# Kernel optimization log

Hardware: AMD Instinct MI355X
Metric: run time of the kernel (lower is better)

The kernel has to match this reference:

```python
import jax, jax.numpy as jnp
import numpy as np

N_NODES = 50000
N_EDGES = 800000
IN_CH = 128
HID = 32
HEADS = 4
OUT_CH = 64
N_GRAPHS = 64


def setup_inputs() -> dict:
    key = jax.random.key(0)
    ks = jax.random.split(key, 16)
    x = jax.random.normal(ks[0], (N_NODES, IN_CH), dtype=jnp.float32)
    edge_index = jax.random.randint(ks[1], (2, N_EDGES), 0, N_NODES, dtype=jnp.int64)
    edge_attr = jax.random.normal(ks[2], (N_EDGES, 8), dtype=jnp.float32)
    nodeIDs = jnp.sort(jax.random.randint(ks[3], (N_NODES,), 0, N_GRAPHS, dtype=jnp.int64))
    s = 0.1
    W1 = jax.random.normal(ks[4], (IN_CH, HEADS * HID), dtype=jnp.float32) * s
    att_src1 = jax.random.normal(ks[5], (HEADS, HID), dtype=jnp.float32) * s
    att_dst1 = jax.random.normal(ks[6], (HEADS, HID), dtype=jnp.float32) * s
    b1 = jax.random.normal(ks[7], (HEADS * HID,), dtype=jnp.float32) * s
    W2 = jax.random.normal(ks[8], (HEADS * HID, 16), dtype=jnp.float32) * s
    att_src2 = jax.random.normal(ks[9], (1, 16), dtype=jnp.float32) * s
    att_dst2 = jax.random.normal(ks[10], (1, 16), dtype=jnp.float32) * s
    b2 = jax.random.normal(ks[11], (16,), dtype=jnp.float32) * s
    Wf = jax.random.normal(ks[12], (16, OUT_CH), dtype=jnp.float32) * s
    bf = jax.random.normal(ks[13], (OUT_CH,), dtype=jnp.float32) * s
    return dict(x=x, edge_index=edge_index, edge_attr=edge_attr, nodeIDs=nodeIDs,
                W1=W1, att_src1=att_src1, att_dst1=att_dst1, b1=b1,
                W2=W2, att_src2=att_src2, att_dst2=att_dst2, b2=b2,
                Wf=Wf, bf=bf)


def gat_conv(x, src, dst, n, W, a_src, a_dst, b, heads, out_ch, concat):
    # linear transform -> [N, H, C]
    h = (x @ W).reshape(n, heads, out_ch)
    # per-node attention logits [N, H]
    asrc = jnp.sum(h * a_src, axis=-1)
    adst = jnp.sum(h * a_dst, axis=-1)
    e = jax.nn.leaky_relu(asrc[src] + adst[dst], 0.2)  # [E, H]
    # segment softmax over edges sharing the same destination node
    m = jax.ops.segment_max(e, dst, num_segments=n)
    e = jnp.exp(e - m[dst])
    s = jax.ops.segment_sum(e, dst, num_segments=n)
    alpha = e / (s[dst] + 1e-16)
    # weighted scatter-add aggregation: [N, H, C]
    out = jax.ops.segment_sum(alpha[:, :, None] * h[src], dst, num_segments=n)
    out = out.reshape(n, heads * out_ch) if concat else out.mean(axis=1)
    return out + b


def reference(x, edge_index, edge_attr, nodeIDs, W1, att_src1, att_dst1, b1,
              W2, att_src2, att_dst2, b2, Wf, bf):
    n = x.shape[0]
    # GATConv default: add self-loops
    loop = jnp.arange(n, dtype=edge_index.dtype)
    src = jnp.concatenate([edge_index[0], loop])
    dst = jnp.concatenate([edge_index[1], loop])
    # eval mode: dropout is identity. edge_attr ignored (no edge_dim in GATConv).
    h = jax.nn.relu(gat_conv(x, src, dst, n, W1, att_src1, att_dst1, b1, HEADS, HID, True))
    h = jax.nn.relu(gat_conv(h, src, dst, n, W2, att_src2, att_dst2, b2, 1, 16, False))
    # global mean pool over graphs
    sums = jax.ops.segment_sum(h, nodeIDs, num_segments=N_GRAPHS)
    cnts = jax.ops.segment_sum(jnp.ones((n,), dtype=h.dtype), nodeIDs, num_segments=N_GRAPHS)
    pooled = sums / jnp.maximum(cnts, 1.0)[:, None]  # [G, 16]
    return pooled @ Wf + bf
```

## Files before the change

### kernel.cpp

```cpp
#include <hip/hip_runtime.h>
#include <hip/hip_bf16.h>


__device__ __forceinline__ float lrelu02(float x) { return x > 0.f ? x : 0.2f * x; }

__device__ __forceinline__ unsigned short f2bf(float f) {
    unsigned b = __float_as_uint(f);
    return (unsigned short)((b + 0x7fffu + ((b >> 16) & 1u)) >> 16);
}
__device__ __forceinline__ float bf_lo(unsigned u) { return __uint_as_float(u << 16); }
__device__ __forceinline__ float bf_hi(unsigned u) { return __uint_as_float(u & 0xffff0000u); }

typedef __attribute__((ext_vector_type(8))) short short8v;
typedef __attribute__((ext_vector_type(4))) float f32x4;

#define CAP 64

__global__ __launch_bounds__(128) void k_prep(
    const float* __restrict__ W1, unsigned short* __restrict__ W1tb)
{
    int n = blockIdx.x, k = threadIdx.x;
    W1tb[n * 128 + k] = f2bf(W1[k * 128 + n]);
}

__global__ __launch_bounds__(256) void k_gemm1h(
    const float* __restrict__ x, const unsigned short* __restrict__ W1tb,
    const float* __restrict__ a_src, const float* __restrict__ a_dst,
    unsigned short* __restrict__ H1b, float* __restrict__ asrcv, float* __restrict__ adstv, int N,
    const int* __restrict__ src, const int* __restrict__ dst,
    int* __restrict__ cnt, unsigned short* __restrict__ bkt, int E, int GB)
{
    if ((int)blockIdx.x >= GB) {
        const int g  = blockIdx.x & 7;
        const int lo = (int)(((long long)N * g) >> 3);
        const int hi = (int)(((long long)N * (g + 1)) >> 3);
        const int bi = (blockIdx.x - GB) >> 3;
        for (int i = bi * 256 + threadIdx.x; i < E; i += 128 * 256) {
            int d = dst[i];
            if (d >= lo && d < hi) {
                int slot = atomicAdd(&cnt[d], 1);
                if (slot < CAP) bkt[(d << 6) + slot] = (unsigned short)src[i];
            }
        }
        return;
    }

    __shared__ unsigned short sL[4][16][136];
    const int tid = threadIdx.x;
    const int w  = tid >> 6, l = tid & 63;
    const int mr = l & 15, kg = l >> 4;
    const int m0 = w * 16;
    const int rowbase = blockIdx.x * 64;

    const int grow_a = rowbase + m0 + mr;
    const float* xr = x + (size_t)(grow_a < N ? grow_a : N - 1) * 128;

    f32x4 acc[8];
#pragma unroll
    for (int nt = 0; nt < 8; ++nt) acc[nt] = (f32x4){0.f, 0.f, 0.f, 0.f};

#pragma unroll
    for (int kk = 0; kk < 4; ++kk) {
        const int kbase = kk * 32 + kg * 8;
        float4 xa = *(const float4*)(xr + kbase);
        float4 xb = *(const float4*)(xr + kbase + 4);
        short8v a;
        unsigned* ap = (unsigned*)&a;
        ap[0] = (unsigned)f2bf(xa.x) | ((unsigned)f2bf(xa.y) << 16);
        ap[1] = (unsigned)f2bf(xa.z) | ((unsigned)f2bf(xa.w) << 16);
        ap[2] = (unsigned)f2bf(xb.x) | ((unsigned)f2bf(xb.y) << 16);
        ap[3] = (unsigned)f2bf(xb.z) | ((unsigned)f2bf(xb.w) << 16);
#pragma unroll
        for (int nt = 0; nt < 8; ++nt) {
            short8v b = *(const short8v*)&W1tb[(size_t)(nt * 16 + mr) * 128 + kbase];
            acc[nt] = __builtin_amdgcn_mfma_f32_16x16x32_bf16(a, b, acc[nt], 0, 0, 0);
        }
    }

    {
        float as_[8], ad_[8];
#pragma unroll
        for (int nt = 0; nt < 8; ++nt) { as_[nt] = a_src[nt * 16 + mr]; ad_[nt] = a_dst[nt * 16 + mr]; }
#pragma unroll
        for (int j = 0; j < 4; ++j) {
            float vs[4], vd[4];
#pragma unroll
            for (int h = 0; h < 4; ++h) {
                vs[h] = acc[2 * h][j] * as_[2 * h] + acc[2 * h + 1][j] * as_[2 * h + 1];
                vd[h] = acc[2 * h][j] * ad_[2 * h] + acc[2 * h + 1][j] * ad_[2 * h + 1];
#pragma unroll
                for (int xm = 1; xm <= 8; xm <<= 1) {
                    vs[h] += __shfl_xor(vs[h], xm);
                    vd[h] += __shfl_xor(vd[h], xm);
                }
            }
            int grow = rowbase + m0 + kg * 4 + j;
            if (mr == 0 && grow < N) {
                *(float4*)&asrcv[grow * 4] = make_float4(vs[0], vs[1], vs[2], vs[3]);
                *(float4*)&adstv[grow * 4] = make_float4(vd[0], vd[1], vd[2], vd[3]);
            }
        }
    }

#pragma unroll
    for (int nt = 0; nt < 8; ++nt)
#pragma unroll
        for (int j = 0; j < 4; ++j)
            sL[w][kg * 4 + j][nt * 16 + mr] = f2bf(acc[nt][j]);
    {
        int r = l >> 2, k0 = (l & 3) * 32;
        int grow = rowbase + m0 + r;
        if (grow < N) {
            const uint4* sp = (const uint4*)&sL[w][r][k0];
            uint4* dp = (uint4*)&H1b[(size_t)grow * 128 + k0];
#pragma unroll
            for (int q = 0; q < 4; ++q) dp[q] = sp[q];
        }
    }
}

__global__ __launch_bounds__(256) void k_gemm2(
    const float* __restrict__ X, const float* __restrict__ b1,
    const float* __restrict__ W2, const float* __restrict__ a_src2, const float* __restrict__ a_dst2,
    unsigned short* __restrict__ H2b, float* __restrict__ asrcv, float* __restrict__ adstv, int N)
{
    __shared__ float xs[64][132];
    __shared__ float ws[128][16];
    const int tid = threadIdx.x;
    const int rowbase = blockIdx.x * 64;
    {
        int k = tid >> 1, c0 = (tid & 1) * 8;
        *(float4*)&ws[k][c0]     = *(const float4*)&W2[k * 16 + c0];
        *(float4*)&ws[k][c0 + 4] = *(const float4*)&W2[k * 16 + c0 + 4];
    }
    {
        int r = tid >> 2, k0 = (tid & 3) * 32;
        int grow = rowbase + r;
        const float* xp = X + (size_t)(grow < N ? grow : N - 1) * 128 + k0;
#pragma unroll
        for (int q = 0; q < 8; ++q) {
            float4 v  = *(const float4*)(xp + q * 4);
            float4 bb = *(const float4*)&b1[k0 + q * 4];
            xs[r][k0 + q*4 + 0] = fmaxf(v.x + bb.x, 0.f);
            xs[r][k0 + q*4 + 1] = fmaxf(v.y + bb.y, 0.f);
            xs[r][k0 + q*4 + 2] = fmaxf(v.z + bb.z, 0.f);
            xs[r][k0 + q*4 + 3] = fmaxf(v.w + bb.w, 0.f);
        }
    }
    __syncthreads();
    const int r = tid >> 2, c0 = (tid & 3) * 4;
    float acc[4] = {0.f, 0.f, 0.f, 0.f};
#pragma unroll 16
    for (int k = 0; k < 128; ++k) {
        float xv = xs[r][k];
        float4 w = *(const float4*)&ws[k][c0];
        acc[0] = fmaf(xv, w.x, acc[0]);
        acc[1] = fmaf(xv, w.y, acc[1]);
        acc[2] = fmaf(xv, w.z, acc[2]);
        acc[3] = fmaf(xv, w.w, acc[3]);
    }
    int grow = rowbase + r;
    const float4 as4 = *(const float4*)&a_src2[c0];
    const float4 ad4 = *(const float4*)&a_dst2[c0];
    float vs = acc[0]*as4.x + acc[1]*as4.y + acc[2]*as4.z + acc[3]*as4.w;
    float vd = acc[0]*ad4.x + acc[1]*ad4.y + acc[2]*ad4.z + acc[3]*ad4.w;
    vs += __shfl_xor(vs, 1); vd += __shfl_xor(vd, 1);
    vs += __shfl_xor(vs, 2); vd += __shfl_xor(vd, 2);
    if (grow < N) {
        uint2 p;
        p.x = (unsigned)f2bf(acc[0]) | ((unsigned)f2bf(acc[1]) << 16);
        p.y = (unsigned)f2bf(acc[2]) | ((unsigned)f2bf(acc[3]) << 16);
        *(uint2*)&H2b[(size_t)grow * 16 + c0] = p;
        if ((tid & 3) == 0) { asrcv[grow] = vs; adstv[grow] = vd; }
    }
}

__global__ __launch_bounds__(256) void k_agg1(
    const unsigned short* __restrict__ H1b, const float* __restrict__ asrc, const float* __restrict__ adst,
    const int* __restrict__ cnt, const unsigned short* __restrict__ bkt,
    float* __restrict__ out, int N)
{
    __shared__ float sEs[4][64 * 4];
    __shared__ int   sSs[4][64];
    const int w = threadIdx.x >> 6, lane = threadIdx.x & 63;
    float* sE = sEs[w];
    int*   sS = sSs[w];
    const int n = blockIdx.x * 4 + w;
    if (n >= N) return;
    const int deg = min(cnt[n], CAP);

    const float4 ad4 = *(const float4*)&adst[n * 4];
    const float4 as4 = *(const float4*)&asrc[n * 4];
    float es0 = __expf(lrelu02(as4.x + ad4.x));
    float es1 = __expf(lrelu02(as4.y + ad4.y));
    float es2 = __expf(lrelu02(as4.z + ad4.z));
    float es3 = __expf(lrelu02(as4.w + ad4.w));
    float ssum0 = es0, ssum1 = es1, ssum2 = es2, ssum3 = es3;
    if (lane != 0) { ssum0 = 0.f; ssum1 = 0.f; ssum2 = 0.f; ssum3 = 0.f; }

    const int g = lane >> 4, q = lane & 15;
    const int c0 = q * 8, h = q >> 2;
    float acc[8] = {0.f,0.f,0.f,0.f,0.f,0.f,0.f,0.f};

    if (lane < deg) {
        int s = (int)bkt[(n << 6) + lane];
        sS[lane] = s;
        const float4 a = *(const float4*)&asrc[s * 4];
        float e0 = __expf(lrelu02(a.x + ad4.x));
        float e1 = __expf(lrelu02(a.y + ad4.y));
        float e2 = __expf(lrelu02(a.z + ad4.z));
        float e3 = __expf(lrelu02(a.w + ad4.w));
        ssum0 += e0; ssum1 += e1; ssum2 += e2; ssum3 += e3;
        sE[lane * 4 + 0] = e0; sE[lane * 4 + 1] = e1;
        sE[lane * 4 + 2] = e2; sE[lane * 4 + 3] = e3;
    }
    for (int j = g; j < deg; j += 4) {
        int s = sS[j];
        float e = sE[j * 4 + h];
        uint4 u = *(const uint4*)&H1b[(size_t)s * 128 + c0];
        acc[0] = fmaf(e, bf_lo(u.x), acc[0]);
        acc[1] = fmaf(e, bf_hi(u.x), acc[1]);
        acc[2] = fmaf(e, bf_lo(u.y), acc[2]);
        acc[3] = fmaf(e, bf_hi(u.y), acc[3]);
        acc[4] = fmaf(e, bf_lo(u.z), acc[4]);
        acc[5] = fmaf(e, bf_hi(u.z), acc[5]);
        acc[6] = fmaf(e, bf_lo(u.w), acc[6]);
        acc[7] = fmaf(e, bf_hi(u.w), acc[7]);
    }

#pragma unroll
    for (int xm = 32; xm >= 1; xm >>= 1) {
        ssum0 += __shfl_xor(ssum0, xm);
        ssum1 += __shfl_xor(ssum1, xm);
        ssum2 += __shfl_xor(ssum2, xm);
        ssum3 += __shfl_xor(ssum3, xm);
    }
#pragma unroll
    for (int k = 0; k < 8; ++k) {
        acc[k] += __shfl_xor(acc[k], 16);
        acc[k] += __shfl_xor(acc[k], 32);
    }
    if (g == 0) {
        float ssv = (h == 0) ? ssum0 : (h == 1) ? ssum1 : (h == 2) ? ssum2 : ssum3;
        float esv = (h == 0) ? es0   : (h == 1) ? es1   : (h == 2) ? es2   : es3;
        float inv = 1.f / (ssv + 1e-16f);
        uint4 u = *(const uint4*)&H1b[(size_t)n * 128 + c0];
        float o[8];
        o[0] = (acc[0] + esv * bf_lo(u.x)) * inv;
        o[1] = (acc[1] + esv * bf_hi(u.x)) * inv;
        o[2] = (acc[2] + esv * bf_lo(u.y)) * inv;
        o[3] = (acc[3] + esv * bf_hi(u.y)) * inv;
        o[4] = (acc[4] + esv * bf_lo(u.z)) * inv;
        o[5] = (acc[5] + esv * bf_hi(u.z)) * inv;
        o[6] = (acc[6] + esv * bf_lo(u.w)) * inv;
        o[7] = (acc[7] + esv * bf_hi(u.w)) * inv;
        *(float4*)&out[(size_t)n * 128 + c0]     = make_float4(o[0], o[1], o[2], o[3]);
        *(float4*)&out[(size_t)n * 128 + c0 + 4] = make_float4(o[4], o[5], o[6], o[7]);
    }
}

__global__ __launch_bounds__(256) void k_agg2(
    const unsigned short* __restrict__ H2b, const float* __restrict__ asrc, const float* __restrict__ adst,
    const int* __restrict__ cnt, const unsigned short* __restrict__ bkt,
    float* __restrict__ out, int N)
{
    __shared__ float sEs[4][64];
    __shared__ int   sSs[4][64];
    const int w = threadIdx.x >> 6, lane = threadIdx.x & 63;
    float* sE = sEs[w];
    int*   sS = sSs[w];
    const int n = blockIdx.x * 4 + w;
    if (n >= N) return;
    const int deg = min(cnt[n], CAP);

    const float adv = adst[n];
    float eself = __expf(lrelu02(asrc[n] + adv));
    float ssum = (lane == 0) ? eself : 0.f;

    const int g = lane >> 3, q = lane & 7;
    const int c0 = q * 2;
    float acc0 = 0.f, acc1 = 0.f;

    if (lane < deg) {
        int s = (int)bkt[(n << 6) + lane];
        sS[lane] = s;
        float e = __expf(lrelu02(asrc[s] + adv));
        ssum += e;
        sE[lane] = e;
    }
    for (int j = g; j < deg; j += 8) {
        int s = sS[j];
        float e = sE[j];
        unsigned u = *(const unsigned*)&H2b[(size_t)s * 16 + c0];
        acc0 = fmaf(e, bf_lo(u), acc0);
        acc1 = fmaf(e, bf_hi(u), acc1);
    }
#pragma unroll
    for (int xm = 32; xm >= 1; xm >>= 1) ssum += __shfl_xor(ssum, xm);
    acc0 += __shfl_xor(acc0, 8);  acc1 += __shfl_xor(acc1, 8);
    acc0 += __shfl_xor(acc0, 16); acc1 += __shfl_xor(acc1, 16);
    acc0 += __shfl_xor(acc0, 32); acc1 += __shfl_xor(acc1, 32);
    if (g == 0) {
        float inv = 1.f / (ssum + 1e-16f);
        unsigned u = *(const unsigned*)&H2b[(size_t)n * 16 + c0];
        float2 o;
        o.x = (acc0 + eself * bf_lo(u)) * inv;
        o.y = (acc1 + eself * bf_hi(u)) * inv;
        *(float2*)&out[(size_t)n * 16 + c0] = o;
    }
}

__global__ __launch_bounds__(256) void k_poolfinal(
    const float* __restrict__ out2, const float* __restrict__ b2,
    const int* __restrict__ nodeIDs, const float* __restrict__ Wf,
    const float* __restrict__ bf, float* __restrict__ outp, int N)
{
    int g = blockIdx.x;
    int lo = 0, hi = N;
    while (lo < hi) { int mid = (lo + hi) >> 1; if (nodeIDs[mid] < g) lo = mid + 1; else hi = mid; }
    int start = lo;
    lo = 0; hi = N;
    while (lo < hi) { int mid = (lo + hi) >> 1; if (nodeIDs[mid] < g + 1) lo = mid + 1; else hi = mid; }
    int end = lo;

    int c = threadIdx.x & 15, grp = threadIdx.x >> 4;
    float bc = b2[c];
    float acc = 0.f;
    for (int n = start + grp; n < end; n += 16)
        acc += fmaxf(out2[(size_t)n * 16 + c] + bc, 0.f);

    __shared__ float sd[256];
    __shared__ float p16[16];
    sd[threadIdx.x] = acc;
    __syncthreads();
#pragma unroll
    for (int s = 8; s >= 1; s >>= 1) {
        if (grp < s) sd[threadIdx.x] += sd[(grp + s) * 16 + c];
        __syncthreads();
    }
    if (threadIdx.x < 16) {
        float cnt_ = (float)(end - start);
        p16[threadIdx.x] = sd[threadIdx.x] / fmaxf(cnt_, 1.f);
    }
    __syncthreads();
    if (threadIdx.x < 64) {
        int o = threadIdx.x;
        float a = bf[o];
#pragma unroll
        for (int k = 0; k < 16; ++k)
            a = fmaf(p16[k], Wf[k * 64 + o], a);
        outp[(size_t)g * 64 + o] = a;
    }
}

extern "C" void kernel_launch(void* const* d_in, const int* in_sizes, int n_in,
                              void* d_out, int out_size, void* d_ws, size_t ws_size,
                              hipStream_t stream)
{
    const float* x   = (const float*)d_in[0];
    const int*   ei  = (const int*)  d_in[1];
    const int*   nid = (const int*)  d_in[3];
    const float* W1  = (const float*)d_in[4];
    const float* as1 = (const float*)d_in[5];
    const float* ad1 = (const float*)d_in[6];
    const float* b1  = (const float*)d_in[7];
    const float* W2  = (const float*)d_in[8];
    const float* as2 = (const float*)d_in[9];
    const float* ad2 = (const float*)d_in[10];
    const float* b2  = (const float*)d_in[11];
    const float* Wf  = (const float*)d_in[12];
    const float* bf  = (const float*)d_in[13];
    float* outp = (float*)d_out;

    const int N = in_sizes[0] / 128;
    const int E = in_sizes[1] / 2;
    const int* src = ei;
    const int* dst = ei + E;

    char* ws = (char*)d_ws;
    size_t off_b = 0;
    auto alloc = [&](size_t bytes) -> char* {
        char* p = ws + off_b;
        off_b += (bytes + 255) & ~(size_t)255;
        return p;
    };

    unsigned short* H1b  = (unsigned short*)alloc((size_t)N * 128 * 2);
    unsigned short* H2b  = (unsigned short*)alloc((size_t)N * 16 * 2);
    unsigned short* bkt  = (unsigned short*)alloc((size_t)N * CAP * 2);
    unsigned short* W1tb = (unsigned short*)alloc((size_t)128 * 128 * 2);
    float* out1   = (float*)alloc((size_t)N * 128 * 4);
    float* asrc1  = (float*)alloc((size_t)N * 4 * 4);
    float* adst1  = (float*)alloc((size_t)N * 4 * 4);
    float* out2   = (float*)alloc((size_t)N * 16 * 4);
    float* asrc2  = (float*)alloc((size_t)N * 4);
    float* adst2  = (float*)alloc((size_t)N * 4);
    int*   cnt    = (int*)  alloc((size_t)N * 4);

    auto cdiv = [](long long a, long long b) { return (int)((a + b - 1) / b); };

    const int GB = cdiv(N, 64);

    hipMemsetAsync(cnt, 0, (size_t)N * 4, stream);
    k_prep<<<128, 128, 0, stream>>>(W1, W1tb);

    k_gemm1h<<<GB + 1024, 256, 0, stream>>>(x, W1tb, as1, ad1, H1b, asrc1, adst1, N,
                                            src, dst, cnt, bkt, E, GB);

    k_agg1<<<cdiv(N, 4), 256, 0, stream>>>(H1b, asrc1, adst1, cnt, bkt, out1, N);

    k_gemm2<<<cdiv(N, 64), 256, 0, stream>>>(out1, b1, W2, as2, ad2, H2b, asrc2, adst2, N);
    k_agg2<<<cdiv(N, 4), 256, 0, stream>>>(H2b, asrc2, adst2, cnt, bkt, out2, N);

    k_poolfinal<<<out_size / 64, 256, 0, stream>>>(out2, b2, nid, Wf, bf, outp, N);
}
```

Measured before the change: 158.9 us.

## Fuse bias+ReLU into agg1 bf16 output, MFMA layer-2 GEMM, split bucketing kernel

Layer-1 aggregation now applies bias and ReLU itself and writes bf16 instead of fp32, which halves the intermediate traffic. The layer-2 GEMM reads that bf16 buffer and uses MFMA bf16 instructions with a W2 pre-transposed in the prep kernel. Edge bucketing moves out of the GEMM1 kernel into its own launch and uses nontemporal loads, with src loaded only on matching edges. The split removes the overlap between bucketing and GEMM1 and adds a launch. Rounding layer-1 activations to bf16 adds precision loss.

```diff
diff --git a/kernel.cpp b/kernel.cpp
--- a/kernel.cpp
+++ b/kernel.cpp
@@ -17,34 +17,19 @@
 #define CAP 64
 
 __global__ __launch_bounds__(128) void k_prep(
-    const float* __restrict__ W1, unsigned short* __restrict__ W1tb)
-{
-    int n = blockIdx.x, k = threadIdx.x;
-    W1tb[n * 128 + k] = f2bf(W1[k * 128 + n]);
-}
-
-__global__ __launch_bounds__(256) void k_gemm1h(
+    const float* __restrict__ W1, const float* __restrict__ W2,
+    unsigned short* __restrict__ W1tb, unsigned short* __restrict__ W2tb)
+{
+    int b = blockIdx.x, k = threadIdx.x;
+    if (b < 128) W1tb[b * 128 + k] = f2bf(W1[k * 128 + b]);
+    else { int c = b - 128; W2tb[c * 128 + k] = f2bf(W2[k * 16 + c]); }
+}
+
+__global__ __launch_bounds__(256) void k_gemm1(
     const float* __restrict__ x, const unsigned short* __restrict__ W1tb,
     const float* __restrict__ a_src, const float* __restrict__ a_dst,
-    unsigned short* __restrict__ H1b, float* __restrict__ asrcv, float* __restrict__ adstv, int N,
-    const int* __restrict__ src, const int* __restrict__ dst,
-    int* __restrict__ cnt, unsigned short* __restrict__ bkt, int E, int GB)
-{
-    if ((int)blockIdx.x >= GB) {
-        const int g  = blockIdx.x & 7;
-        const int lo = (int)(((long long)N * g) >> 3);
-        const int hi = (int)(((long long)N * (g + 1)) >> 3);
-        const int bi = (blockIdx.x - GB) >> 3;
-        for (int i = bi * 256 + threadIdx.x; i < E; i += 128 * 256) {
-            int d = dst[i];
-            if (d >= lo && d < hi) {
-                int slot = atomicAdd(&cnt[d], 1);
-                if (slot < CAP) bkt[(d << 6) + slot] = (unsigned short)src[i];
-            }
-        }
-        return;
-    }
-
+    unsigned short* __restrict__ H1b, float* __restrict__ asrcv, float* __restrict__ adstv, int N)
+{
     __shared__ unsigned short sL[4][16][136];
     const int tid = threadIdx.x;
     const int w  = tid >> 6, l = tid & 63;
@@ -119,66 +104,29 @@
     }
 }
 
-__global__ __launch_bounds__(256) void k_gemm2(
-    const float* __restrict__ X, const float* __restrict__ b1,
-    const float* __restrict__ W2, const float* __restrict__ a_src2, const float* __restrict__ a_dst2,
-    unsigned short* __restrict__ H2b, float* __restrict__ asrcv, float* __restrict__ adstv, int N)
-{
-    __shared__ float xs[64][132];
-    __shared__ float ws[128][16];
-    const int tid = threadIdx.x;
-    const int rowbase = blockIdx.x * 64;
-    {
-        int k = tid >> 1, c0 = (tid & 1) * 8;
-        *(float4*)&ws[k][c0]     = *(const float4*)&W2[k * 16 + c0];
-        *(float4*)&ws[k][c0 + 4] = *(const float4*)&W2[k * 16 + c0 + 4];
-    }
-    {
-        int r = tid >> 2, k0 = (tid & 3) * 32;
-        int grow = rowbase + r;
-        const float* xp = X + (size_t)(grow < N ? grow : N - 1) * 128 + k0;
-#pragma unroll
-        for (int q = 0; q < 8; ++q) {
-            float4 v  = *(const float4*)(xp + q * 4);
-            float4 bb = *(const float4*)&b1[k0 + q * 4];
-            xs[r][k0 + q*4 + 0] = fmaxf(v.x + bb.x, 0.f);
-            xs[r][k0 + q*4 + 1] = fmaxf(v.y + bb.y, 0.f);
-            xs[r][k0 + q*4 + 2] = fmaxf(v.z + bb.z, 0.f);
-            xs[r][k0 + q*4 + 3] = fmaxf(v.w + bb.w, 0.f);
+__global__ __launch_bounds__(256) void k_bucket(
+    const int* __restrict__ src, const int* __restrict__ dst,
+    int* __restrict__ cnt, unsigned short* __restrict__ bkt, int E, int N)
+{
+    const int g  = blockIdx.x & 7;
+    const int lo = (int)(((long long)N * g) >> 3);
+    const int hi = (int)(((long long)N * (g + 1)) >> 3);
+    const int nb = gridDim.x >> 3;
+    const int bi = blockIdx.x >> 3;
+    for (int i = bi * 256 + threadIdx.x; i < E; i += nb * 256) {
+        int d = __builtin_nontemporal_load(&dst[i]);
+        if (d >= lo && d < hi) {
+            int s = __builtin_nontemporal_load(&src[i]);
+            int slot = atomicAdd(&cnt[d], 1);
+            if (slot < CAP) bkt[(d << 6) + slot] = (unsigned short)s;
         }
-    }
-    __syncthreads();
-    const int r = tid >> 2, c0 = (tid & 3) * 4;
-    float acc[4] = {0.f, 0.f, 0.f, 0.f};
-#pragma unroll 16
-    for (int k = 0; k < 128; ++k) {
-        float xv = xs[r][k];
-        float4 w = *(const float4*)&ws[k][c0];
-        acc[0] = fmaf(xv, w.x, acc[0]);
-        acc[1] = fmaf(xv, w.y, acc[1]);
-        acc[2] = fmaf(xv, w.z, acc[2]);
-        acc[3] = fmaf(xv, w.w, acc[3]);
-    }
-    int grow = rowbase + r;
-    const float4 as4 = *(const float4*)&a_src2[c0];
-    const float4 ad4 = *(const float4*)&a_dst2[c0];
-    float vs = acc[0]*as4.x + acc[1]*as4.y + acc[2]*as4.z + acc[3]*as4.w;
-    float vd = acc[0]*ad4.x + acc[1]*ad4.y + acc[2]*ad4.z + acc[3]*ad4.w;
-    vs += __shfl_xor(vs, 1); vd += __shfl_xor(vd, 1);
-    vs += __shfl_xor(vs, 2); vd += __shfl_xor(vd, 2);
-    if (grow < N) {
-        uint2 p;
-        p.x = (unsigned)f2bf(acc[0]) | ((unsigned)f2bf(acc[1]) << 16);
-        p.y = (unsigned)f2bf(acc[2]) | ((unsigned)f2bf(acc[3]) << 16);
-        *(uint2*)&H2b[(size_t)grow * 16 + c0] = p;
-        if ((tid & 3) == 0) { asrcv[grow] = vs; adstv[grow] = vd; }
     }
 }
 
 __global__ __launch_bounds__(256) void k_agg1(
     const unsigned short* __restrict__ H1b, const float* __restrict__ asrc, const float* __restrict__ adst,
     const int* __restrict__ cnt, const unsigned short* __restrict__ bkt,
-    float* __restrict__ out, int N)
+    const float* __restrict__ b1, unsigned short* __restrict__ out1b, int N)
 {
     __shared__ float sEs[4][64 * 4];
     __shared__ int   sSs[4][64];
@@ -254,8 +202,49 @@
         o[5] = (acc[5] + esv * bf_hi(u.z)) * inv;
         o[6] = (acc[6] + esv * bf_lo(u.w)) * inv;
         o[7] = (acc[7] + esv * bf_hi(u.w)) * inv;
-        *(float4*)&out[(size_t)n * 128 + c0]     = make_float4(o[0], o[1], o[2], o[3]);
-        *(float4*)&out[(size_t)n * 128 + c0 + 4] = make_float4(o[4], o[5], o[6], o[7]);
+        const float4 ba = *(const float4*)&b1[c0];
+        const float4 bb = *(const float4*)&b1[c0 + 4];
+        uint4 pk;
+        pk.x = (unsigned)f2bf(fmaxf(o[0] + ba.x, 0.f)) | ((unsigned)f2bf(fmaxf(o[1] + ba.y, 0.f)) << 16);
+        pk.y = (unsigned)f2bf(fmaxf(o[2] + ba.z, 0.f)) | ((unsigned)f2bf(fmaxf(o[3] + ba.w, 0.f)) << 16);
+        pk.z = (unsigned)f2bf(fmaxf(o[4] + bb.x, 0.f)) | ((unsigned)f2bf(fmaxf(o[5] + bb.y, 0.f)) << 16);
+        pk.w = (unsigned)f2bf(fmaxf(o[6] + bb.z, 0.f)) | ((unsigned)f2bf(fmaxf(o[7] + bb.w, 0.f)) << 16);
+        *(uint4*)&out1b[(size_t)n * 128 + c0] = pk;
+    }
+}
+
+__global__ __launch_bounds__(256) void k_gemm2m(
+    const unsigned short* __restrict__ X1b, const unsigned short* __restrict__ W2tb,
+    const float* __restrict__ a_src2, const float* __restrict__ a_dst2,
+    unsigned short* __restrict__ H2b, float* __restrict__ asrcv, float* __restrict__ adstv, int N)
+{
+    const int tid = threadIdx.x;
+    const int w = tid >> 6, l = tid & 63;
+    const int mr = l & 15, kg = l >> 4;
+    const int rowbase = blockIdx.x * 64 + w * 16;
+    const int grow_a = rowbase + mr;
+    const unsigned short* xr = X1b + (size_t)(grow_a < N ? grow_a : N - 1) * 128;
+
+    f32x4 acc = (f32x4){0.f, 0.f, 0.f, 0.f};
+#pragma unroll
+    for (int kk = 0; kk < 4; ++kk) {
+        const int kbase = kk * 32 + kg * 8;
+        short8v a = *(const short8v*)&xr[kbase];
+        short8v b = *(const short8v*)&W2tb[mr * 128 + kbase];
+        acc = __builtin_amdgcn_mfma_f32_16x16x32_bf16(a, b, acc, 0, 0, 0);
+    }
+    const float as_ = a_src2[mr], ad_ = a_dst2[mr];
+#pragma unroll
+    for (int j = 0; j < 4; ++j) {
+        float vs = acc[j] * as_;
+        float vd = acc[j] * ad_;
+#pragma unroll
+        for (int xm = 1; xm <= 8; xm <<= 1) { vs += __shfl_xor(vs, xm); vd += __shfl_xor(vd, xm); }
+        int grow = rowbase + kg * 4 + j;
+        if (grow < N) {
+            H2b[(size_t)grow * 16 + mr] = f2bf(acc[j]);
+            if (mr == 0) { asrcv[grow] = vs; adstv[grow] = vd; }
+        }
     }
 }
 
@@ -385,11 +374,12 @@
         return p;
     };
 
-    unsigned short* H1b  = (unsigned short*)alloc((size_t)N * 128 * 2);
-    unsigned short* H2b  = (unsigned short*)alloc((size_t)N * 16 * 2);
-    unsigned short* bkt  = (unsigned short*)alloc((size_t)N * CAP * 2);
-    unsigned short* W1tb = (unsigned short*)alloc((size_t)128 * 128 * 2);
-    float* out1   = (float*)alloc((size_t)N * 128 * 4);
+    unsigned short* H1b   = (unsigned short*)alloc((size_t)N * 128 * 2);
+    unsigned short* out1b = (unsigned short*)alloc((size_t)N * 128 * 2);
+    unsigned short* H2b   = (unsigned short*)alloc((size_t)N * 16 * 2);
+    unsigned short* bkt   = (unsigned short*)alloc((size_t)N * CAP * 2);
+    unsigned short* W1tb  = (unsigned short*)alloc((size_t)128 * 128 * 2);
+    unsigned short* W2tb  = (unsigned short*)alloc((size_t)16 * 128 * 2);
     float* asrc1  = (float*)alloc((size_t)N * 4 * 4);
     float* adst1  = (float*)alloc((size_t)N * 4 * 4);
     float* out2   = (float*)alloc((size_t)N * 16 * 4);
@@ -402,14 +392,16 @@
     const int GB = cdiv(N, 64);
 
     hipMemsetAsync(cnt, 0, (size_t)N * 4, stream);
-    k_prep<<<128, 128, 0, stream>>>(W1, W1tb);
-
-    k_gemm1h<<<GB + 1024, 256, 0, stream>>>(x, W1tb, as1, ad1, H1b, asrc1, adst1, N,
-                                            src, dst, cnt, bkt, E, GB);
-
-    k_agg1<<<cdiv(N, 4), 256, 0, stream>>>(H1b, asrc1, adst1, cnt, bkt, out1, N);
-
-    k_gemm2<<<cdiv(N, 64), 256, 0, stream>>>(out1, b1, W2, as2, ad2, H2b, asrc2, adst2, N);
+    k_prep<<<144, 128, 0, stream>>>(W1, W2, W1tb, W2tb);
+
+    k_bucket<<<1024, 256, 0, stream>>>(src, dst, cnt, bkt, E, N);
+
+    k_gemm1<<<GB, 256, 0, stream>>>(x, W1tb, as1, ad1, H1b, asrc1, adst1, N);
+
+    k_agg1<<<cdiv(N, 4), 256, 0, stream>>>(H1b, asrc1, adst1, cnt, bkt, b1, out1b, N);
+
+    k_gemm2m<<<cdiv(N, 64), 256, 0, stream>>>(out1b, W2tb, as2, ad2, H2b, asrc2, adst2, N);
+
     k_agg2<<<cdiv(N, 4), 256, 0, stream>>>(H2b, asrc2, adst2, cnt, bkt, out2, N);
 
     k_poolfinal<<<out_size / 64, 256, 0, stream>>>(out2, b2, nid, Wf, bf, outp, N);
```

After: 169.3 us. 6.6% more time.
